# Kernel tuning notes

Measured on AMD Instinct MI355X. Metric: run time of the kernel, lower is better.

Reference implementation:

```python
import jax, jax.numpy as jnp
import numpy as np

N_NODES = 100000
N_EDGES = 1600000
D_IN = 128
D_OUT = 128


def setup_inputs() -> dict:
    key = jax.random.key(0)
    ks = jax.random.split(key, 8)
    x = jax.random.normal(ks[0], (N_NODES, D_IN), dtype=jnp.float32)
    edge_index = jax.random.randint(ks[1], (2, N_EDGES), 0, N_NODES, dtype=jnp.int64)
    s1 = 1.0 / np.sqrt(D_IN)
    s2 = 1.0 / np.sqrt(D_OUT)
    # SAGEConv: lin_l acts on aggregated neighbors (has bias), lin_r on self (no bias)
    Wl1 = jax.random.uniform(ks[2], (D_OUT, D_IN), jnp.float32, -s1, s1)
    Wr1 = jax.random.uniform(ks[3], (D_OUT, D_IN), jnp.float32, -s1, s1)
    b1 = jnp.zeros((D_OUT,), jnp.float32)
    Wl2 = jax.random.uniform(ks[4], (D_OUT, D_OUT), jnp.float32, -s2, s2)
    Wr2 = jax.random.uniform(ks[5], (D_OUT, D_OUT), jnp.float32, -s2, s2)
    b2 = jnp.zeros((D_OUT,), jnp.float32)
    return {"x": x, "edge_index": edge_index, "Wl1": Wl1, "Wr1": Wr1, "b1": b1,
            "Wl2": Wl2, "Wr2": Wr2, "b2": b2}


def _sage_conv(x, src, dst, Wl, Wr, b, n_nodes):
    # mean aggregation of source features at destination nodes
    agg = jax.ops.segment_sum(x[src], dst, num_segments=n_nodes)  # [N, d]
    deg = jax.ops.segment_sum(jnp.ones((src.shape[0],), x.dtype), dst, num_segments=n_nodes)
    mean = agg / jnp.maximum(deg, 1.0)[:, None]  # isolated nodes -> 0 (PyG scatter-mean)
    return mean @ Wl.T + b + x @ Wr.T


def reference(x, edge_index, Wl1, Wr1, b1, Wl2, Wr2, b2):
    src, dst = edge_index[0], edge_index[1]
    n = x.shape[0]
    h = _sage_conv(x, src, dst, Wl1, Wr1, b1, n)
    h = _sage_conv(h, src, dst, Wl2, Wr2, b2, n)
    return h
```

## Files before the change

### kernel.cpp

```cpp
#include <hip/hip_runtime.h>
#include <hip/hip_bf16.h>

#define D 128
#define SCAN_CHUNK 1024
#define TE 4096

typedef __attribute__((ext_vector_type(8))) short bf16x8;
typedef __attribute__((ext_vector_type(4))) float f32x4;
typedef __attribute__((ext_vector_type(2))) float f32x2;

__device__ __forceinline__ bool ei_is64(const int* ei32) {
    return (ei32[1] | ei32[3] | ei32[5] | ei32[7]) == 0;
}
__device__ __forceinline__ int get_idx(const void* ei, bool is64, long long pos) {
    return is64 ? (int)((const long long*)ei)[pos] : ((const int*)ei)[pos];
}

__global__ __launch_bounds__(256) void prep_kernel(
    const float* __restrict__ x, unsigned* __restrict__ xq, long long ND, int ncvt,
    const float* __restrict__ Wl1, const float* __restrict__ Wr1,
    const float* __restrict__ Wl2, const float* __restrict__ Wr2,
    ushort* __restrict__ Wf1, ushort* __restrict__ Wf2,
    const void* __restrict__ ei, int E, int NB, int NBLK, int SH,
    int* __restrict__ histT) {
    __shared__ int h[512];
    const int t = threadIdx.x;
    int bid = blockIdx.x;

    if (bid < ncvt) {
        long long i = ((long long)bid * 256 + t) * 8;
        if (i + 7 < ND) {
            float4 v0 = *reinterpret_cast<const float4*>(x + i);
            float4 v1 = *reinterpret_cast<const float4*>(x + i + 4);
            int p0 = __builtin_amdgcn_cvt_pk_fp8_f32(v0.x, v0.y, 0, false);
            p0 = __builtin_amdgcn_cvt_pk_fp8_f32(v0.z, v0.w, p0, true);
            int p1 = __builtin_amdgcn_cvt_pk_fp8_f32(v1.x, v1.y, 0, false);
            p1 = __builtin_amdgcn_cvt_pk_fp8_f32(v1.z, v1.w, p1, true);
            *reinterpret_cast<uint2*>(reinterpret_cast<unsigned char*>(xq) + i) =
                make_uint2((unsigned)p0, (unsigned)p1);
        } else {
            for (; i < ND; ++i) {
                int pk = __builtin_amdgcn_cvt_pk_fp8_f32(x[i], x[i], 0, false);
                reinterpret_cast<unsigned char*>(xq)[i] = (unsigned char)(pk & 0xff);
            }
        }
        return;
    }
    bid -= ncvt;
    if (bid < 32) {
        int gid = bid * 256 + t;
        int id = gid & 4095;
        const float* Wl = Wl1; const float* Wr = Wr1; ushort* Wf = Wf1;
        if (gid >= 4096) { Wl = Wl2; Wr = Wr2; Wf = Wf2; }
        int lane = id & 63, s = (id >> 6) & 7, j = id >> 9;
        int c = j * 16 + (lane & 15);
        int k = s * 32 + ((lane >> 4) << 3);
        const float* src = (k < 128) ? (Wl + c * 128 + k) : (Wr + c * 128 + (k - 128));
        float4 v0 = *reinterpret_cast<const float4*>(src);
        float4 v1 = *reinterpret_cast<const float4*>(src + 4);
        __hip_bfloat16 o[8];
        o[0] = __float2bfloat16(v0.x); o[1] = __float2bfloat16(v0.y);
        o[2] = __float2bfloat16(v0.z); o[3] = __float2bfloat16(v0.w);
        o[4] = __float2bfloat16(v1.x); o[5] = __float2bfloat16(v1.y);
        o[6] = __float2bfloat16(v1.z); o[7] = __float2bfloat16(v1.w);
        *reinterpret_cast<uint4*>(Wf + (size_t)id * 8) = *reinterpret_cast<uint4*>(o);
        return;
    }
    bid -= 32;
    for (int b = t; b < 512; b += 256) h[b] = 0;
    bool is64 = ei_is64((const int*)ei);
    __syncthreads();
    const int base = bid * TE;
    for (int i = t; i < TE; i += 256) {
        int e = base + i;
        if (e < E) {
            int d = get_idx(ei, is64, (long long)E + e);
            atomicAdd(&h[d >> SH], 1);
        }
    }
    __syncthreads();
    for (int b = t; b < NB; b += 256) histT[b * NBLK + bid] = h[b];
}

__global__ __launch_bounds__(256) void scan_partial_kernel(int* __restrict__ arr, int Ntot,
                                                           int* __restrict__ bsum) {
    __shared__ int s[SCAN_CHUNK];
    int base = blockIdx.x * SCAN_CHUNK;
    for (int j = threadIdx.x; j < SCAN_CHUNK; j += 256) {
        int i = base + j;
        s[j] = (i < Ntot) ? arr[i] : 0;
    }
    __syncthreads();
    if (threadIdx.x == 0) {
        int run = 0;
        for (int j = 0; j < SCAN_CHUNK; ++j) { int t = s[j]; s[j] = run; run += t; }
        bsum[blockIdx.x] = run;
    }
    __syncthreads();
    for (int j = threadIdx.x; j < SCAN_CHUNK; j += 256) {
        int i = base + j;
        if (i < Ntot) arr[i] = s[j];
    }
}

__global__ __launch_bounds__(256) void scan_top_kernel(int* __restrict__ bsum, int nb) {
    __shared__ int s[1024];
    const int t = threadIdx.x;
    for (int j = t; j < nb; j += 256) s[j] = bsum[j];
    __syncthreads();
    if (t == 0) {
        int run = 0;
        for (int j = 0; j < nb; ++j) { int v = s[j]; s[j] = run; run += v; }
    }
    __syncthreads();
    for (int j = t; j < nb; j += 256) bsum[j] = s[j];
}

__global__ __launch_bounds__(256) void part_scatter_kernel(const void* __restrict__ ei, int E,
                                                           int NB, int NBLK, int SH,
                                                           const int* __restrict__ histT,
                                                           const int* __restrict__ bsum,
                                                           unsigned* __restrict__ ebuf) {
    __shared__ int cur[512];
    const int t = threadIdx.x;
    bool is64 = ei_is64((const int*)ei);
    for (int b = t; b < NB; b += 256) {
        int idx = b * NBLK + blockIdx.x;
        cur[b] = histT[idx] + bsum[idx >> 10];
    }
    __syncthreads();
    const int base = blockIdx.x * TE;
    for (int i = t; i < TE; i += 256) {
        int e = base + i;
        if (e < E) {
            int s = get_idx(ei, is64, e);
            int d = get_idx(ei, is64, (long long)E + e);
            int pos = atomicAdd(&cur[d >> SH], 1);
            ebuf[pos] = (unsigned)s | ((unsigned)(d & ((1 << SH) - 1)) << 24);
        }
    }
}

__global__ __launch_bounds__(256) void bucket_csr_kernel(const unsigned* __restrict__ ebuf,
                                                         const int* __restrict__ histT,
                                                         const int* __restrict__ bsum,
                                                         int NB, int NBLK, int SH, int E,
                                                         int N, int* __restrict__ rs,
                                                         int* __restrict__ col) {
    const int b = blockIdx.x, t = threadIdx.x;
    const int nodes = 1 << SH;
    __shared__ int h[256];
    __shared__ int cur[256];
    __shared__ int sse[2];
    if (t == 0) {
        int i0 = b * NBLK;
        sse[0] = histT[i0] + bsum[i0 >> 10];
        if (b + 1 < NB) {
            int i1 = (b + 1) * NBLK;
            sse[1] = histT[i1] + bsum[i1 >> 10];
        } else {
            sse[1] = E;
        }
    }
    for (int l = t; l < nodes; l += 256) h[l] = 0;
    __syncthreads();
    const int bstart = sse[0], bend = sse[1];
    for (int i = bstart + t; i < bend; i += 256) {
        atomicAdd(&h[ebuf[i] >> 24], 1);
    }
    __syncthreads();
    for (int off = 1; off < nodes; off <<= 1) {
        int v = 0;
        if (t < nodes && t >= off) v = h[t - off];
        __syncthreads();
        if (t < nodes && t >= off) h[t] += v;
        __syncthreads();
    }
    const int node0 = b << SH;
    if (t < nodes) {
        int node = node0 + t;
        if (node < N) rs[node] = bstart + h[t];
        cur[t] = bstart + (t ? h[t - 1] : 0);
    }
    __syncthreads();
    for (int i = bstart + t; i < bend; i += 256) {
        unsigned ed = ebuf[i];
        int pos = atomicAdd(&cur[ed >> 24], 1);
        col[pos] = (int)(ed & 0xFFFFFFu);
    }
}

__global__ __launch_bounds__(256) void aggregate_mean_fp8_kernel(
    const unsigned char* __restrict__ xq, const int* __restrict__ rs,
    const int* __restrict__ col, ushort* __restrict__ outm, int N) {
    const int t = threadIdx.x;
    const int v = blockIdx.x * 16 + (t >> 4);
    if (v >= N) return;
    const int lc = t & 15;
    const int start = v ? rs[v - 1] : 0, end = rs[v];
    const unsigned char* xbase = xq + lc * 8;
    f32x2 a0 = {0.f, 0.f}, a1 = {0.f, 0.f}, a2 = {0.f, 0.f}, a3 = {0.f, 0.f};
    int e = start;
    for (; e + 3 < end; e += 4) {
        int s0 = col[e], s1 = col[e + 1], s2 = col[e + 2], s3 = col[e + 3];
        uint2 d0 = *reinterpret_cast<const uint2*>(xbase + (size_t)s0 * D);
        uint2 d1 = *reinterpret_cast<const uint2*>(xbase + (size_t)s1 * D);
        uint2 d2 = *reinterpret_cast<const uint2*>(xbase + (size_t)s2 * D);
        uint2 d3 = *reinterpret_cast<const uint2*>(xbase + (size_t)s3 * D);
        a0 += __builtin_amdgcn_cvt_pk_f32_fp8((int)d0.x, false);
        a1 += __builtin_amdgcn_cvt_pk_f32_fp8((int)d0.x, true);
        a2 += __builtin_amdgcn_cvt_pk_f32_fp8((int)d0.y, false);
        a3 += __builtin_amdgcn_cvt_pk_f32_fp8((int)d0.y, true);
        a0 += __builtin_amdgcn_cvt_pk_f32_fp8((int)d1.x, false);
        a1 += __builtin_amdgcn_cvt_pk_f32_fp8((int)d1.x, true);
        a2 += __builtin_amdgcn_cvt_pk_f32_fp8((int)d1.y, false);
        a3 += __builtin_amdgcn_cvt_pk_f32_fp8((int)d1.y, true);
        a0 += __builtin_amdgcn_cvt_pk_f32_fp8((int)d2.x, false);
        a1 += __builtin_amdgcn_cvt_pk_f32_fp8((int)d2.x, true);
        a2 += __builtin_amdgcn_cvt_pk_f32_fp8((int)d2.y, false);
        a3 += __builtin_amdgcn_cvt_pk_f32_fp8((int)d2.y, true);
        a0 += __builtin_amdgcn_cvt_pk_f32_fp8((int)d3.x, false);
        a1 += __builtin_amdgcn_cvt_pk_f32_fp8((int)d3.x, true);
        a2 += __builtin_amdgcn_cvt_pk_f32_fp8((int)d3.y, false);
        a3 += __builtin_amdgcn_cvt_pk_f32_fp8((int)d3.y, true);
    }
    for (; e < end; ++e) {
        int s0 = col[e];
        uint2 d0 = *reinterpret_cast<const uint2*>(xbase + (size_t)s0 * D);
        a0 += __builtin_amdgcn_cvt_pk_f32_fp8((int)d0.x, false);
        a1 += __builtin_amdgcn_cvt_pk_f32_fp8((int)d0.x, true);
        a2 += __builtin_amdgcn_cvt_pk_f32_fp8((int)d0.y, false);
        a3 += __builtin_amdgcn_cvt_pk_f32_fp8((int)d0.y, true);
    }
    float inv = (end > start) ? 1.0f / (float)(end - start) : 0.f;
    __hip_bfloat16 o[8];
    o[0] = __float2bfloat16(a0.x * inv); o[1] = __float2bfloat16(a0.y * inv);
    o[2] = __float2bfloat16(a1.x * inv); o[3] = __float2bfloat16(a1.y * inv);
    o[4] = __float2bfloat16(a2.x * inv); o[5] = __float2bfloat16(a2.y * inv);
    o[6] = __float2bfloat16(a3.x * inv); o[7] = __float2bfloat16(a3.y * inv);
    *reinterpret_cast<uint4*>(outm + (size_t)v * D + lc * 8) =
        *reinterpret_cast<uint4*>(o);
}

template <typename OutT, bool DUAL, bool SELFF32>
__global__ __launch_bounds__(512) void sage_mfma_kernel(
    const ushort* __restrict__ Ab, const void* __restrict__ Sb,
    const ushort* __restrict__ Wf, const float* __restrict__ bias,
    OutT* __restrict__ out, unsigned char* __restrict__ fq, int N) {
    __shared__ uint4 ldsB[4096];
    const int t = threadIdx.x;
    {
        const uint4* g = reinterpret_cast<const uint4*>(Wf);
#pragma unroll
        for (int i = 0; i < 8; ++i) ldsB[t + i * 512] = g[t + i * 512];
    }
    __syncthreads();

    const int lane = t & 63, w = t >> 6;
    const int lm = lane & 15;
    const int ksub = (lane >> 4) * 8;
    const int mbase = blockIdx.x * 128 + w * 16;

    int r0 = mbase + lm;
    if (r0 >= N) r0 = N - 1;

    f32x4 acc[8];
#pragma unroll
    for (int j = 0; j < 8; ++j) {
        float bv = bias[j * 16 + lm];
        acc[j] = {bv, bv, bv, bv};
    }

    const ushort* A0 = Ab + (size_t)r0 * D + ksub;
    const ushort* lB = reinterpret_cast<const ushort*>(ldsB) + lane * 8;

#pragma unroll
    for (int s = 0; s < 8; ++s) {
        bf16x8 a;
        if (s < 4) {
            a = *reinterpret_cast<const bf16x8*>(A0 + s * 32);
        } else if constexpr (SELFF32) {
            const float* S0 = (const float*)Sb + (size_t)r0 * D + (s - 4) * 32 + ksub;
            float4 v0 = *reinterpret_cast<const float4*>(S0);
            float4 v1 = *reinterpret_cast<const float4*>(S0 + 4);
            __hip_bfloat16 o[8];
            o[0] = __float2bfloat16(v0.x); o[1] = __float2bfloat16(v0.y);
            o[2] = __float2bfloat16(v0.z); o[3] = __float2bfloat16(v0.w);
            o[4] = __float2bfloat16(v1.x); o[5] = __float2bfloat16(v1.y);
            o[6] = __float2bfloat16(v1.z); o[7] = __float2bfloat16(v1.w);
            a = *reinterpret_cast<bf16x8*>(o);
        } else {
            const ushort* S0 = (const ushort*)Sb + (size_t)r0 * D + ksub;
            a = *reinterpret_cast<const bf16x8*>(S0 + (s - 4) * 32);
        }
#pragma unroll
        for (int j = 0; j < 8; ++j) {
            bf16x8 b = *reinterpret_cast<const bf16x8*>(lB + (j * 8 + s) * 512);
            acc[j] = __builtin_amdgcn_mfma_f32_16x16x32_bf16(a, b, acc[j], 0, 0, 0);
        }
    }

    const int rr = (lane >> 4) * 4;
#pragma unroll
    for (int r = 0; r < 4; ++r) {
        int row = mbase + rr + r;
        if (row < N) {
#pragma unroll
            for (int j = 0; j < 8; ++j) {
                float val = acc[j][r];
                if constexpr (sizeof(OutT) == 2)
                    out[(size_t)row * D + j * 16 + lm] = __float2bfloat16(val);
                else
                    out[(size_t)row * D + j * 16 + lm] = val;
                if constexpr (DUAL) {
                    int pk = __builtin_amdgcn_cvt_pk_fp8_f32(val, val, 0, false);
                    fq[(size_t)row * D + j * 16 + lm] = (unsigned char)(pk & 0xff);
                }
            }
        }
    }
}

extern "C" void kernel_launch(void* const* d_in, const int* in_sizes, int n_in,
                              void* d_out, int out_size, void* d_ws, size_t ws_size,
                              hipStream_t stream) {
    const float* x   = (const float*)d_in[0];
    const void*  ei  = d_in[1];
    const float* Wl1 = (const float*)d_in[2];
    const float* Wr1 = (const float*)d_in[3];
    const float* b1  = (const float*)d_in[4];
    const float* Wl2 = (const float*)d_in[5];
    const float* Wr2 = (const float*)d_in[6];
    const float* b2  = (const float*)d_in[7];
    float* out = (float*)d_out;

    const int N = in_sizes[0] / D;
    const int E = in_sizes[1] / 2;
    const long long ND = (long long)N * D;

    int SH = 8;
    while (((N + (1 << SH) - 1) >> SH) > 512) ++SH;
    const int NB = (N + (1 << SH) - 1) >> SH;
    const int NBLK = (E + TE - 1) / TE;
    const int Ntot = NB * NBLK;
    const int nb2 = (Ntot + SCAN_CHUNK - 1) / SCAN_CHUNK;

    ushort* meanb = (ushort*)d_ws;
    ushort* h1b   = meanb + ND;
    ushort* Wf1   = h1b + ND;
    ushort* Wf2   = Wf1 + 32768;
    int*    rs    = (int*)(Wf2 + 32768);
    int*    col   = rs + N;
    int*      histT = (int*)meanb;
    int*      bsum  = histT + Ntot;
    unsigned* ebuf  = (unsigned*)h1b;
    unsigned char* xq  = (unsigned char*)d_out;
    unsigned char* h1q = (unsigned char*)d_out + ND;

    const int ncvt = (int)((ND / 8 + 255) / 256);

    prep_kernel<<<ncvt + 32 + NBLK, 256, 0, stream>>>(
        x, (unsigned*)xq, ND, ncvt, Wl1, Wr1, Wl2, Wr2,
        Wf1, Wf2, ei, E, NB, NBLK, SH, histT);

    scan_partial_kernel<<<nb2, 256, 0, stream>>>(histT, Ntot, bsum);
    scan_top_kernel<<<1, 256, 0, stream>>>(bsum, nb2);
    part_scatter_kernel<<<NBLK, 256, 0, stream>>>(ei, E, NB, NBLK, SH, histT, bsum, ebuf);
    bucket_csr_kernel<<<NB, 256, 0, stream>>>(ebuf, histT, bsum, NB, NBLK, SH, E, N, rs, col);

    const int agg_grid = (N + 15) / 16;
    const int gemm_grid = (N + 127) / 128;

    aggregate_mean_fp8_kernel<<<agg_grid, 256, 0, stream>>>(xq, rs, col, meanb, N);
    sage_mfma_kernel<__hip_bfloat16, true, true><<<gemm_grid, 512, 0, stream>>>(
        meanb, x, Wf1, b1, (__hip_bfloat16*)h1b, h1q, N);

    aggregate_mean_fp8_kernel<<<agg_grid, 256, 0, stream>>>(h1q, rs, col, meanb, N);
    sage_mfma_kernel<float, false, false><<<gemm_grid, 512, 0, stream>>>(
        meanb, h1b, Wf2, b2, out, nullptr, N);
}
```

Before: 180.2 us.

## Parallelize chunk scans and fold top-level scan into consumer kernels

Replaces the serial single-thread chunk scan with a vectorized int4 load plus a Hillis-Steele block scan. It removes the separate top-level scan launch by having part_scatter and bucket_csr each rescan the block sums in LDS. This cuts one kernel launch and serial latency in CSR construction. The aggregation kernel also switches to 32-bit unsigned offset arithmetic for gathers. The redundant per-block bsum scan assumes nb2 <= 256 and SH == 8.

```diff
diff --git a/kernel.cpp b/kernel.cpp
--- a/kernel.cpp
+++ b/kernel.cpp
@@ -84,49 +84,67 @@
 
 __global__ __launch_bounds__(256) void scan_partial_kernel(int* __restrict__ arr, int Ntot,
                                                            int* __restrict__ bsum) {
-    __shared__ int s[SCAN_CHUNK];
-    int base = blockIdx.x * SCAN_CHUNK;
-    for (int j = threadIdx.x; j < SCAN_CHUNK; j += 256) {
-        int i = base + j;
-        s[j] = (i < Ntot) ? arr[i] : 0;
-    }
-    __syncthreads();
-    if (threadIdx.x == 0) {
-        int run = 0;
-        for (int j = 0; j < SCAN_CHUNK; ++j) { int t = s[j]; s[j] = run; run += t; }
-        bsum[blockIdx.x] = run;
-    }
-    __syncthreads();
-    for (int j = threadIdx.x; j < SCAN_CHUNK; j += 256) {
-        int i = base + j;
-        if (i < Ntot) arr[i] = s[j];
-    }
-}
-
-__global__ __launch_bounds__(256) void scan_top_kernel(int* __restrict__ bsum, int nb) {
-    __shared__ int s[1024];
-    const int t = threadIdx.x;
-    for (int j = t; j < nb; j += 256) s[j] = bsum[j];
-    __syncthreads();
-    if (t == 0) {
-        int run = 0;
-        for (int j = 0; j < nb; ++j) { int v = s[j]; s[j] = run; run += v; }
-    }
-    __syncthreads();
-    for (int j = t; j < nb; j += 256) bsum[j] = s[j];
+    __shared__ int ws[256];
+    const int t = threadIdx.x;
+    const int i0 = blockIdx.x * SCAN_CHUNK + t * 4;
+    int4 v = {0, 0, 0, 0};
+    if (i0 + 3 < Ntot) {
+        v = *reinterpret_cast<const int4*>(arr + i0);
+    } else {
+        if (i0 < Ntot) v.x = arr[i0];
+        if (i0 + 1 < Ntot) v.y = arr[i0 + 1];
+        if (i0 + 2 < Ntot) v.z = arr[i0 + 2];
+        if (i0 + 3 < Ntot) v.w = arr[i0 + 3];
+    }
+    ws[t] = v.x + v.y + v.z + v.w;
+    __syncthreads();
+    for (int off = 1; off < 256; off <<= 1) {
+        int val = (t >= off) ? ws[t - off] : 0;
+        __syncthreads();
+        ws[t] += val;
+        __syncthreads();
+    }
+    int ex = t ? ws[t - 1] : 0;
+    int e0 = ex, e1 = ex + v.x, e2 = e1 + v.y, e3 = e2 + v.z;
+    if (i0 + 3 < Ntot) {
+        *reinterpret_cast<int4*>(arr + i0) = make_int4(e0, e1, e2, e3);
+    } else {
+        if (i0 < Ntot) arr[i0] = e0;
+        if (i0 + 1 < Ntot) arr[i0 + 1] = e1;
+        if (i0 + 2 < Ntot) arr[i0 + 2] = e2;
+        if (i0 + 3 < Ntot) arr[i0 + 3] = e3;
+    }
+    if (t == 255) bsum[blockIdx.x] = ws[255];
+}
+
+__device__ __forceinline__ void scan_bsum_lds(const int* __restrict__ bsum, int nb2,
+                                              int* sb) {
+    const int t = threadIdx.x;
+    sb[t] = (t < nb2) ? bsum[t] : 0;
+    __syncthreads();
+    for (int off = 1; off < 256; off <<= 1) {
+        int v = (t >= off) ? sb[t - off] : 0;
+        __syncthreads();
+        sb[t] += v;
+        __syncthreads();
+    }
 }
 
 __global__ __launch_bounds__(256) void part_scatter_kernel(const void* __restrict__ ei, int E,
                                                            int NB, int NBLK, int SH,
                                                            const int* __restrict__ histT,
                                                            const int* __restrict__ bsum,
+                                                           int nb2,
                                                            unsigned* __restrict__ ebuf) {
     __shared__ int cur[512];
+    __shared__ int sb[256];
     const int t = threadIdx.x;
     bool is64 = ei_is64((const int*)ei);
+    scan_bsum_lds(bsum, nb2, sb);
     for (int b = t; b < NB; b += 256) {
         int idx = b * NBLK + blockIdx.x;
-        cur[b] = histT[idx] + bsum[idx >> 10];
+        int c = idx >> 10;
+        cur[b] = histT[idx] + (c ? sb[c - 1] : 0);
     }
     __syncthreads();
     const int base = blockIdx.x * TE;
@@ -144,6 +162,7 @@
 __global__ __launch_bounds__(256) void bucket_csr_kernel(const unsigned* __restrict__ ebuf,
                                                          const int* __restrict__ histT,
                                                          const int* __restrict__ bsum,
+                                                         int nb2,
                                                          int NB, int NBLK, int SH, int E,
                                                          int N, int* __restrict__ rs,
                                                          int* __restrict__ col) {
@@ -151,18 +170,22 @@
     const int nodes = 1 << SH;
     __shared__ int h[256];
     __shared__ int cur[256];
+    __shared__ int sb[256];
     __shared__ int sse[2];
+    scan_bsum_lds(bsum, nb2, sb);
     if (t == 0) {
         int i0 = b * NBLK;
-        sse[0] = histT[i0] + bsum[i0 >> 10];
+        int c0 = i0 >> 10;
+        sse[0] = histT[i0] + (c0 ? sb[c0 - 1] : 0);
         if (b + 1 < NB) {
             int i1 = (b + 1) * NBLK;
-            sse[1] = histT[i1] + bsum[i1 >> 10];
+            int c1 = i1 >> 10;
+            sse[1] = histT[i1] + (c1 ? sb[c1 - 1] : 0);
         } else {
             sse[1] = E;
         }
     }
-    for (int l = t; l < nodes; l += 256) h[l] = 0;
+    h[t] = 0;
     __syncthreads();
     const int bstart = sse[0], bend = sse[1];
     for (int i = bstart + t; i < bend; i += 256) {
@@ -170,14 +193,13 @@
     }
     __syncthreads();
     for (int off = 1; off < nodes; off <<= 1) {
-        int v = 0;
-        if (t < nodes && t >= off) v = h[t - off];
-        __syncthreads();
-        if (t < nodes && t >= off) h[t] += v;
+        int v = (t >= off) ? h[t - off] : 0;
+        __syncthreads();
+        h[t] += v;
         __syncthreads();
     }
     const int node0 = b << SH;
-    if (t < nodes) {
+    {
         int node = node0 + t;
         if (node < N) rs[node] = bstart + h[t];
         cur[t] = bstart + (t ? h[t - 1] : 0);
@@ -196,17 +218,19 @@
     const int t = threadIdx.x;
     const int v = blockIdx.x * 16 + (t >> 4);
     if (v >= N) return;
-    const int lc = t & 15;
+    const unsigned lcoff = (unsigned)(t & 15) * 8u;
     const int start = v ? rs[v - 1] : 0, end = rs[v];
-    const unsigned char* xbase = xq + lc * 8;
     f32x2 a0 = {0.f, 0.f}, a1 = {0.f, 0.f}, a2 = {0.f, 0.f}, a3 = {0.f, 0.f};
     int e = start;
     for (; e + 3 < end; e += 4) {
-        int s0 = col[e], s1 = col[e + 1], s2 = col[e + 2], s3 = col[e + 3];
-        uint2 d0 = *reinterpret_cast<const uint2*>(xbase + (size_t)s0 * D);
-        uint2 d1 = *reinterpret_cast<const uint2*>(xbase + (size_t)s1 * D);
-        uint2 d2 = *reinterpret_cast<const uint2*>(xbase + (size_t)s2 * D);
-        uint2 d3 = *reinterpret_cast<const uint2*>(xbase + (size_t)s3 * D);
+        unsigned o0 = ((unsigned)col[e] << 7) + lcoff;
+        unsigned o1 = ((unsigned)col[e + 1] << 7) + lcoff;
+        unsigned o2 = ((unsigned)col[e + 2] << 7) + lcoff;
+        unsigned o3 = ((unsigned)col[e + 3] << 7) + lcoff;
+        uint2 d0 = *reinterpret_cast<const uint2*>(xq + o0);
+        uint2 d1 = *reinterpret_cast<const uint2*>(xq + o1);
+        uint2 d2 = *reinterpret_cast<const uint2*>(xq + o2);
+        uint2 d3 = *reinterpret_cast<const uint2*>(xq + o3);
         a0 += __builtin_amdgcn_cvt_pk_f32_fp8((int)d0.x, false);
         a1 += __builtin_amdgcn_cvt_pk_f32_fp8((int)d0.x, true);
         a2 += __builtin_amdgcn_cvt_pk_f32_fp8((int)d0.y, false);
@@ -225,8 +249,8 @@
         a3 += __builtin_amdgcn_cvt_pk_f32_fp8((int)d3.y, true);
     }
     for (; e < end; ++e) {
-        int s0 = col[e];
-        uint2 d0 = *reinterpret_cast<const uint2*>(xbase + (size_t)s0 * D);
+        unsigned o0 = ((unsigned)col[e] << 7) + lcoff;
+        uint2 d0 = *reinterpret_cast<const uint2*>(xq + o0);
         a0 += __builtin_amdgcn_cvt_pk_f32_fp8((int)d0.x, false);
         a1 += __builtin_amdgcn_cvt_pk_f32_fp8((int)d0.x, true);
         a2 += __builtin_amdgcn_cvt_pk_f32_fp8((int)d0.y, false);
@@ -238,7 +262,7 @@
     o[2] = __float2bfloat16(a1.x * inv); o[3] = __float2bfloat16(a1.y * inv);
     o[4] = __float2bfloat16(a2.x * inv); o[5] = __float2bfloat16(a2.y * inv);
     o[6] = __float2bfloat16(a3.x * inv); o[7] = __float2bfloat16(a3.y * inv);
-    *reinterpret_cast<uint4*>(outm + (size_t)v * D + lc * 8) =
+    *reinterpret_cast<uint4*>(outm + (size_t)v * D + ((t & 15) << 3)) =
         *reinterpret_cast<uint4*>(o);
 }
 
@@ -364,9 +388,8 @@
         Wf1, Wf2, ei, E, NB, NBLK, SH, histT);
 
     scan_partial_kernel<<<nb2, 256, 0, stream>>>(histT, Ntot, bsum);
-    scan_top_kernel<<<1, 256, 0, stream>>>(bsum, nb2);
-    part_scatter_kernel<<<NBLK, 256, 0, stream>>>(ei, E, NB, NBLK, SH, histT, bsum, ebuf);
-    bucket_csr_kernel<<<NB, 256, 0, stream>>>(ebuf, histT, bsum, NB, NBLK, SH, E, N, rs, col);
+    part_scatter_kernel<<<NBLK, 256, 0, stream>>>(ei, E, NB, NBLK, SH, histT, bsum, nb2, ebuf);
+    bucket_csr_kernel<<<NB, 256, 0, stream>>>(ebuf, histT, bsum, nb2, NB, NBLK, SH, E, N, rs, col);
 
     const int agg_grid = (N + 15) / 16;
     const int gemm_grid = (N + 127) / 128;
```

Result: faster. 170.0 us (-5.7%).
